# Kernel tuning notes

Hardware: AMD Instinct MI355X
Metric: run time of the kernel (lower is better)

Reference implementation:

```python
import jax, jax.numpy as jnp
import numpy as np

IMG = 160      # img_size
P = 100        # img_pathch_num = (160/16)^2
NBLK = 256     # pixels per 16x16 patch
NCLS = 4

def _index_matrix():
    # faithful port of NewAIFV.index_init
    ind = np.arange(256)
    start = (ind // 16) * IMG + (ind % 16) * 16
    idx = np.zeros(NBLK * P, dtype=np.int32)
    for i in range(P):
        idx[i * 256:(i + 1) * 256] = start + (i // 16) * 16 * IMG + (i % 16)
    return jnp.asarray(idx)

_IDX = _index_matrix()


def setup_inputs() -> dict:
    key = jax.random.key(0)
    ks = jax.random.split(key, 7)
    B, C = 4, 256
    return {
        "feat_S": jax.random.normal(ks[0], (B, C, IMG, IMG), jnp.float32),
        "feat_T": jax.random.normal(ks[1], (B, C, IMG, IMG), jnp.float32),
        "Pred_S": jax.random.normal(ks[2], (B, NCLS, IMG, IMG), jnp.float32),
        "Pred_T": jax.random.normal(ks[3], (B, NCLS, IMG, IMG), jnp.float32),
        "S_atten": jax.random.normal(ks[4], (B, P, P), jnp.float32),
        "T_atten": jax.random.normal(ks[5], (B, P, P), jnp.float32),
        "target": jax.random.randint(ks[6], (B, 1, IMG, IMG), 0, NCLS, jnp.int32),
    }


def _cos(a, b):
    # torch.nn.CosineSimilarity(dim=1): dot / max(|a||b|, 1e-8)
    num = (a * b).sum(1)
    den = jnp.maximum(jnp.sqrt((a * a).sum(1)) * jnp.sqrt((b * b).sum(1)), 1e-8)
    return num / den


def reference(feat_S, feat_T, Pred_S, Pred_T, S_atten, T_atten, target):
    B, C, H, W = feat_S.shape
    hw = H * W
    idx = _IDX
    # gathered patch reorder (index_select along flattened spatial dim)
    fS = feat_S.reshape(B, C, hw)[:, :, idx]
    fT = feat_T.reshape(B, C, hw)[:, :, idx]
    tg = target.reshape(B, 1, hw)[:, :, idx].reshape(B, 1, H, W)
    # 256-iteration loop of per-patch [B,C,100]@[B,100,100] matmuls -> one einsum
    TS = jnp.einsum('bcik,bkj->bcij', fS.reshape(B, C, NBLK, P), S_atten).reshape(B, C, H, W)
    TT = jnp.einsum('bcik,bkj->bcij', fT.reshape(B, C, NBLK, P), T_atten).reshape(B, C, H, W)
    ScS = jax.nn.softmax(Pred_S, axis=1).reshape(B, NCLS, hw)[:, :, idx].reshape(B, NCLS, H, W)
    ScT = jax.nn.softmax(Pred_T, axis=1).reshape(B, NCLS, hw)[:, :, idx].reshape(B, NCLS, H, W)
    dt = TS.dtype
    one_hot = (tg == jnp.arange(NCLS)[None, :, None, None]).astype(dt)   # [B,4,H,W]
    wei_s = (ScS * one_hot).sum(1)  # [B,H,W]
    wei_t = (ScT * one_hot).sum(1)
    tf = tg.astype(dt)  # [B,1,H,W], broadcast replaces nn.Upsample+expand

    def centers(class_list, s_prto, t_prto, eps):
        cS, cT = TS, TT
        for i in range(NCLS):
            j = class_list[i]
            stmp = ScT[:, j:j + 1]              # [B,1,H,W] (Score_Tmp, broadcast over C)
            m = (tf == i).astype(dt)            # mask_feat (class i)
            mp = (tf == j).astype(dt)           # mask_feat_prto (class class_list[i])
            denS = (mp if s_prto else m).sum((-1, -2)) + eps          # [B,1]
            protoS = ((mp * TS).sum((-1, -2)) / denS)[:, :, None, None]
            denT = (stmp * (mp if t_prto else m)).sum((-1, -2)) + eps
            protoT = ((mp * TT * stmp).sum((-1, -2)) / denT)[:, :, None, None]
            cS = (1 - m) * cS + m * protoS
            cT = (1 - m) * cT + m * protoT
        return cS, cT

    # three variants exactly as in the torch loops (denominator choices differ)
    cS0, cT0 = centers([1, 0, 3, 2], False, False, 1e-6)
    cS1, cT1 = centers([2, 3, 0, 1], True, True, 1e-6)
    cS2, cT2 = centers([3, 2, 1, 0], True, True, 1.0)

    w = (1 - wei_s) * wei_t
    vec_s = jnp.stack([w * _cos(TS, c) for c in (cS0, cS1, cS2)], axis=1)  # [B,3,H,W]
    vec_t = jnp.stack([w * _cos(TT, c) for c in (cT0, cT1, cT2)], axis=1)
    return jnp.mean((vec_s - vec_t) ** 2)
```

## Files before the change

kernel.cpp:

```cpp
#include <hip/hip_runtime.h>
#include <cstdint>
#include <cstddef>

#define HW 25600

typedef __attribute__((ext_vector_type(8))) short bf16x8;
typedef __attribute__((ext_vector_type(16))) float f32x16;

union ABu { bf16x8 v; uint2 u[2]; };
union B128 { bf16x8 v; int4 q; };

__device__ __forceinline__ f32x16 zero16() {
    f32x16 z;
#pragma unroll
    for (int i = 0; i < 16; ++i) z[i] = 0.f;
    return z;
}

__device__ __forceinline__ unsigned short f2bf(float x) {
    unsigned u = __builtin_bit_cast(unsigned, x);
    unsigned r = (u + 0x7FFF + ((u >> 16) & 1)) >> 16;
    return (unsigned short)r;
}

__device__ __forceinline__ float bf2f(unsigned short s) {
    return __builtin_bit_cast(float, (unsigned)s << 16);
}

__device__ __forceinline__ float wred(float v) {
#pragma unroll
    for (int off = 32; off; off >>= 1) v += __shfl_down(v, off, 64);
    return v;
}

__device__ double blockReduce256D(double v, double* s4) {
#pragma unroll
    for (int off = 32; off; off >>= 1) v += __shfl_down(v, off, 64);
    __syncthreads();
    if ((threadIdx.x & 63) == 0) s4[threadIdx.x >> 6] = v;
    __syncthreads();
    return s4[0] + s4[1] + s4[2] + s4[3];
}

__global__ __launch_bounds__(256) void k1_prep(
    const float* __restrict__ PredS, const float* __restrict__ PredT,
    const int* __restrict__ target,
    int* __restrict__ cls_arr, float* __restrict__ wT_arr,
    float* __restrict__ w_arr, float* __restrict__ partial_prep)
{
    __shared__ float sL[4][20];
    int blk = blockIdx.x;
    int b = blk / 100, r = blk - b * 100;
    int t = threadIdx.x, w = t >> 6, lane = t & 63;
    int ql = r * 256 + t;
    int v = ((t >> 4) * 160) + ((t & 15) * 16) + ((r >> 4) * 2560) + (r & 15);

    int cls = target[b * HW + v];

    const float* pS = PredS + b * 4 * HW + v;
    float a0 = pS[0], a1 = pS[HW], a2 = pS[2 * HW], a3 = pS[3 * HW];
    float mS = fmaxf(fmaxf(a0, a1), fmaxf(a2, a3));
    float e0 = expf(a0 - mS), e1 = expf(a1 - mS), e2 = expf(a2 - mS), e3 = expf(a3 - mS);
    float invS = 1.0f / (e0 + e1 + e2 + e3);
    float wei_s = ((cls == 0) ? e0 : (cls == 1) ? e1 : (cls == 2) ? e2 : e3) * invS;

    const float* pT = PredT + b * 4 * HW + v;
    float c0 = pT[0], c1 = pT[HW], c2 = pT[2 * HW], c3 = pT[3 * HW];
    float mT = fmaxf(fmaxf(c0, c1), fmaxf(c2, c3));
    float f0 = expf(c0 - mT), f1 = expf(c1 - mT), f2 = expf(c2 - mT), f3 = expf(c3 - mT);
    float invT = 1.0f / (f0 + f1 + f2 + f3);
    float tn0 = f0 * invT, tn1 = f1 * invT, tn2 = f2 * invT, tn3 = f3 * invT;
    float wei_t = (cls == 0) ? tn0 : (cls == 1) ? tn1 : (cls == 2) ? tn2 : tn3;

    cls_arr[b * HW + ql] = cls;
    wT_arr[b * HW + ql] = wei_t;
    w_arr[b * HW + ql] = (1.0f - wei_s) * wei_t;

    float vals[20];
#pragma unroll
    for (int s = 0; s < 4; ++s) vals[s] = (cls == s) ? 1.f : 0.f;
#pragma unroll
    for (int i2 = 0; i2 < 4; ++i2) {
        vals[4 + i2 * 4 + 0] = (cls == i2) ? tn0 : 0.f;
        vals[4 + i2 * 4 + 1] = (cls == i2) ? tn1 : 0.f;
        vals[4 + i2 * 4 + 2] = (cls == i2) ? tn2 : 0.f;
        vals[4 + i2 * 4 + 3] = (cls == i2) ? tn3 : 0.f;
    }
#pragma unroll
    for (int s = 0; s < 20; ++s) {
        float rv = wred(vals[s]);
        if (lane == 0) sL[w][s] = rv;
    }
    __syncthreads();
    if (t < 20) {
        int ob = blk * 20;
        partial_prep[ob + t] = sL[0][t] + sL[1][t] + sL[2][t] + sL[3][t];
    }
}

__global__ __launch_bounds__(128) void k2_w(
    const float* __restrict__ Satt, const float* __restrict__ Tatt,
    const int* __restrict__ cls_arr, const float* __restrict__ wT_arr,
    unsigned short* __restrict__ Wbf_S, unsigned short* __restrict__ Wbf_T,
    const float* __restrict__ partial_prep, float* __restrict__ cnt, float* __restrict__ E)
{
    int blk = blockIdx.x;
    int t = threadIdx.x;
    if (blk >= 1024) {
        int i = blk - 1024;
        if (t < 64) {
            int b = i / 20, s = i - (i / 20) * 20;
            float a = partial_prep[(b * 100 + t) * 20 + s];
            if (t + 64 < 100) a += partial_prep[(b * 100 + t + 64) * 20 + s];
            a = wred(a);
            if (t == 0) { if (s < 4) cnt[b * 4 + s] = a; else E[b * 16 + (s - 4)] = a; }
        }
        return;
    }
    __shared__ float Al[100 * 101];
    __shared__ int cls_s[100];
    __shared__ float wTs[100];
    int b = blk >> 8, i = blk & 255;
    if (t < 100) {
        cls_s[t] = cls_arr[b * HW + i * 100 + t];
        wTs[t] = wT_arr[b * HW + i * 100 + t];
    }
    for (int f = t; f < 10000; f += 128) Al[f + f / 100] = Satt[b * 10000 + f];
    __syncthreads();
    if (t < 100) {
        float a0 = 0, a1 = 0, a2 = 0, a3 = 0;
        for (int jc = 0; jc < 100; ++jc) {
            float a = Al[t * 101 + jc];
            int cc = cls_s[jc];
            a0 += (cc == 0) ? a : 0.f;
            a1 += (cc == 1) ? a : 0.f;
            a2 += (cc == 2) ? a : 0.f;
            a3 += (cc == 3) ? a : 0.f;
        }
        uint2 pk;
        pk.x = (unsigned)f2bf(a0) | ((unsigned)f2bf(a1) << 16);
        pk.y = (unsigned)f2bf(a2) | ((unsigned)f2bf(a3) << 16);
        *(uint2*)(Wbf_S + (size_t)(b * HW + i * 100 + t) * 4) = pk;
    }
    __syncthreads();
    for (int f = t; f < 10000; f += 128) Al[f + f / 100] = Tatt[b * 10000 + f];
    __syncthreads();
    if (t < 100) {
        float a0 = 0, a1 = 0, a2 = 0, a3 = 0;
        for (int jc = 0; jc < 100; ++jc) {
            float a = Al[t * 101 + jc] * wTs[jc];
            int cc = cls_s[jc];
            a0 += (cc == 0) ? a : 0.f;
            a1 += (cc == 1) ? a : 0.f;
            a2 += (cc == 2) ? a : 0.f;
            a3 += (cc == 3) ? a : 0.f;
        }
        uint2 pk;
        pk.x = (unsigned)f2bf(a0) | ((unsigned)f2bf(a1) << 16);
        pk.y = (unsigned)f2bf(a2) | ((unsigned)f2bf(a3) << 16);
        *(uint2*)(Wbf_T + (size_t)(b * HW + i * 100 + t) * 4) = pk;
    }
}

__global__ __launch_bounds__(256) void k3_scan(
    const float* __restrict__ featS, const float* __restrict__ featT,
    const unsigned short* __restrict__ WbfS, const unsigned short* __restrict__ WbfT,
    unsigned short* __restrict__ featP, float* __restrict__ pp)
{
    __shared__ unsigned short ldsW[16 * 260 + 8];
    __shared__ float sL[16];
    int x = blockIdx.x;
    int side = x & 1;
    int rest = x >> 1;
    int cq = rest & 63;
    int bd = rest >> 6;
    int D = bd % 7, b = bd / 7;
    int t = threadIdx.x, w = t >> 6, lane = t & 63;

    const float* feat = side ? featT : featS;
    const unsigned short* Wbf = side ? WbfT : WbfS;
    unsigned short* fP = featP + (size_t)side * 26214400u;
    int ppbase = side * 28672 + ((b * 7 + D) * 256) * 4;

    int nr = (D < 6) ? 2 : 1;
    bool act = !(D == 6 && t >= 128);

    int4 w4[2][4];
#pragma unroll
    for (int rep = 0; rep < 2; ++rep) {
        if (rep < nr && act) {
            int Pb = D * 4096 + rep * 2048 + t * 8;
            const int4* wp = (const int4*)(Wbf + ((size_t)b * HW + Pb) * 4);
            w4[rep][0] = wp[0]; w4[rep][1] = wp[1]; w4[rep][2] = wp[2]; w4[rep][3] = wp[3];
        }
    }

    for (int cv = 0; cv < 4; ++cv) {
        int c = cq * 4 + cv;
        const float* fbase = feat + (size_t)(b * 256 + c) * HW + 2560 * D;
#pragma unroll
        for (int ra = 0; ra < 4; ++ra) {
            int A = (t >> 6) + 4 * ra;
            int f4i = t & 63;
            float4 fx = *(const float4*)(fbase + 160 * A + 4 * f4i);
            uint2 pk;
            pk.x = (unsigned)f2bf(fx.x) | ((unsigned)f2bf(fx.y) << 16);
            pk.y = (unsigned)f2bf(fx.z) | ((unsigned)f2bf(fx.w) << 16);
            *(uint2*)(ldsW + A * 260 + 4 * f4i) = pk;
        }
        __syncthreads();

        float as0 = 0.f, as1 = 0.f, as2 = 0.f, as3 = 0.f;
        if (act) {
#pragma unroll
            for (int rep = 0; rep < 2; ++rep) {
                if (rep < nr) {
                    int Pb = D * 4096 + rep * 2048 + t * 8;
                    int A2 = (t & 31) >> 1;
                    int base_unit = A2 * 260 + 128 * (t & 1) + rep * 8 + (t >> 5);
                    unsigned short us[8];
                    float fv[8];
#pragma unroll
                    for (int e = 0; e < 8; ++e) {
                        us[e] = ldsW[base_unit + 16 * e];
                        fv[e] = bf2f(us[e]);
                    }
                    const unsigned short* ww = (const unsigned short*)w4[rep];
#pragma unroll
                    for (int e = 0; e < 8; ++e) {
                        as0 += fv[e] * bf2f(ww[e * 4 + 0]);
                        as1 += fv[e] * bf2f(ww[e * 4 + 1]);
                        as2 += fv[e] * bf2f(ww[e * 4 + 2]);
                        as3 += fv[e] * bf2f(ww[e * 4 + 3]);
                    }
                    int4 outp;
                    ((unsigned*)&outp)[0] = (unsigned)us[0] | ((unsigned)us[1] << 16);
                    ((unsigned*)&outp)[1] = (unsigned)us[2] | ((unsigned)us[3] << 16);
                    ((unsigned*)&outp)[2] = (unsigned)us[4] | ((unsigned)us[5] << 16);
                    ((unsigned*)&outp)[3] = (unsigned)us[6] | ((unsigned)us[7] << 16);
                    *(int4*)(fP + (size_t)(b * 256 + c) * HW + Pb) = outp;
                }
            }
        }

        float rv0 = wred(as0), rv1 = wred(as1), rv2 = wred(as2), rv3 = wred(as3);
        if (lane == 0) {
            sL[w * 4 + 0] = rv0; sL[w * 4 + 1] = rv1;
            sL[w * 4 + 2] = rv2; sL[w * 4 + 3] = rv3;
        }
        __syncthreads();
        if (t < 4) pp[ppbase + c * 4 + t] = sL[t] + sL[4 + t] + sL[8 + t] + sL[12 + t];
        __syncthreads();
    }
}

__global__ void k35_red(const float* __restrict__ pp, float* __restrict__ SumAll)
{
    int id = blockIdx.x * 256 + threadIdx.x;
    int side = id >> 12;
    int rem = id & 4095;
    int bc = rem >> 2, j = rem & 3;
    int b = bc >> 8, c = bc & 255;
    float a = 0.f;
    for (int D = 0; D < 7; ++D)
        a += pp[side * 28672 + (((b * 7 + D) * 256) + c) * 4 + j];
    SumAll[side * 4096 + bc * 4 + j] = a;
}

__global__ __launch_bounds__(256, 2) void k4_mfma(
    const unsigned short* __restrict__ featP,
    const float* __restrict__ SattG, const float* __restrict__ TattG,
    const float* __restrict__ SumAll,
    float* __restrict__ n2S, float* __restrict__ n2T,
    float* __restrict__ dotS, float* __restrict__ dotT)
{
    __shared__ __align__(16) unsigned short featL[32 * 408 + 16];
    __shared__ __align__(16) unsigned short attL[100 * 136];

    int x = blockIdx.x;
    int side = x & 1, chalf = (x >> 1) & 1, b = (x >> 2) & 3, g = x >> 4;
    int t = threadIdx.x, w = t >> 6, l = t & 63;

    const float* Att = side ? TattG : SattG;
    const float* Sum = SumAll + side * 4096;
    const unsigned short* fP = featP + (size_t)side * 26214400u;
    float* n2h = side ? n2T : n2S;
    float* doth = side ? dotT : dotS;

    for (int f = t; f < 13600; f += 256) attL[f] = 0;
    featL[(t >> 3) * 408 + 400 + (t & 7)] = 0;
    if (t < 16) featL[32 * 408 + t] = 0;
    __syncthreads();
    for (int f = t; f < 10000; f += 256) {
        int k = f / 100, j = f - k * 100;
        attL[j * 136 + k] = f2bf(Att[b * 10000 + f]);
    }
    __syncthreads();

    int lj = l & 31, lh = l >> 5;
    bf16x8 breg[7][4];
    {
        int j3 = 96 + lj; if (j3 > 99) j3 = 99;
        int rowoff[4] = { lj, 32 + lj, 64 + lj, j3 };
#pragma unroll
        for (int ks = 0; ks < 7; ++ks)
#pragma unroll
            for (int s = 0; s < 4; ++s)
                breg[ks][s] = ((const B128*)(attL + rowoff[s] * 136 + lh * 8 + ks * 16))->v;
    }

    float n2a[4] = {0, 0, 0, 0};
    float dota[4][4] = {};
    const unsigned short* arow = featL + lj * 408 + w * 100 + lh * 8;

#pragma unroll 1
    for (int ch = 0; ch < 4; ++ch) {
        __syncthreads();
        {
            const unsigned short* src = fP + (size_t)(b * 256 + chalf * 128 + ch * 32 + (t >> 3)) * HW
                                        + g * 400 + (t & 7) * 8;
            unsigned short* dst = featL + (t >> 3) * 408 + (t & 7) * 8;
#pragma unroll
            for (int i = 0; i < 7; ++i) {
                int cb = (t & 7) + i * 8;
                if (cb < 50)
                    *(int4*)(dst + i * 64) = *(const int4*)(src + i * 64);
            }
        }
        __syncthreads();

        f32x16 acc0 = zero16(), acc1 = zero16(), acc2 = zero16(), acc3 = zero16();
#pragma unroll
        for (int ks = 0; ks < 7; ++ks) {
            ABu aF;
            aF.u[0] = *(const uint2*)(arow + ks * 16);
            aF.u[1] = *(const uint2*)(arow + ks * 16 + 4);
            acc0 = __builtin_amdgcn_mfma_f32_32x32x16_bf16(aF.v, breg[ks][0], acc0, 0, 0, 0);
            acc1 = __builtin_amdgcn_mfma_f32_32x32x16_bf16(aF.v, breg[ks][1], acc1, 0, 0, 0);
            acc2 = __builtin_amdgcn_mfma_f32_32x32x16_bf16(aF.v, breg[ks][2], acc2, 0, 0, 0);
            acc3 = __builtin_amdgcn_mfma_f32_32x32x16_bf16(aF.v, breg[ks][3], acc3, 0, 0, 0);
        }

        int cb0 = chalf * 128 + ch * 32 + (lh << 2);
#pragma unroll
        for (int r = 0; r < 16; ++r) {
            int cl = (r & 3) + ((r >> 2) << 3);
            float4 sv = *(const float4*)(Sum + (size_t)(b * 256 + cb0 + cl) * 4);
            float v;
            v = acc0[r]; n2a[0] += v * v;
            dota[0][0] += v * sv.x; dota[0][1] += v * sv.y; dota[0][2] += v * sv.z; dota[0][3] += v * sv.w;
            v = acc1[r]; n2a[1] += v * v;
            dota[1][0] += v * sv.x; dota[1][1] += v * sv.y; dota[1][2] += v * sv.z; dota[1][3] += v * sv.w;
            v = acc2[r]; n2a[2] += v * v;
            dota[2][0] += v * sv.x; dota[2][1] += v * sv.y; dota[2][2] += v * sv.z; dota[2][3] += v * sv.w;
            v = acc3[r]; n2a[3] += v * v;
            dota[3][0] += v * sv.x; dota[3][1] += v * sv.y; dota[3][2] += v * sv.z; dota[3][3] += v * sv.w;
        }
    }

#pragma unroll
    for (int nt = 0; nt < 4; ++nt) {
        n2a[nt] += __shfl_down(n2a[nt], 32, 64);
#pragma unroll
        for (int m = 0; m < 4; ++m) dota[nt][m] += __shfl_down(dota[nt][m], 32, 64);
    }
    if (l < 32) {
        int i0 = g * 4 + w;
        int pqb = b * HW + i0 * 100;
#pragma unroll
        for (int nt = 0; nt < 4; ++nt) {
            int j = nt * 32 + l;
            if (j < 100) {
                n2h[chalf * 102400 + pqb + j] = n2a[nt];
                float4 dv = {dota[nt][0], dota[nt][1], dota[nt][2], dota[nt][3]};
                *(float4*)(doth + chalf * 409600 + (size_t)(pqb + j) * 4) = dv;
            }
        }
    }
}

__global__ void k45_tbl(const float* __restrict__ SumTS, const float* __restrict__ SumTT,
                        const float* __restrict__ cnt, const float* __restrict__ E,
                        float* __restrict__ tbl)
{
    int blk = blockIdx.x, t = threadIdx.x;
    if (blk < 32) {
        int b = blk >> 3, sj = blk & 7, stv = sj >> 2, j = sj & 3;
        const float* S = stv ? SumTT : SumTS;
        float s = 0.f;
#pragma unroll
        for (int u = 0; u < 4; ++u) {
            float xx = S[(b * 256 + t * 4 + u) * 4 + j];
            s += xx * xx;
        }
        s = wred(s);
        if (t == 0) tbl[b * 32 + stv * 4 + j] = sqrtf(s);
    } else if (t < 16) {
        int b = t >> 2, i = t & 3;
        tbl[b * 32 + 8 + 0 * 4 + i] = cnt[b * 4 + i] + 1e-6f;
        tbl[b * 32 + 8 + 1 * 4 + i] = cnt[b * 4 + (i ^ 2)] + 1e-6f;
        tbl[b * 32 + 8 + 2 * 4 + i] = cnt[b * 4 + (i ^ 3)] + 1.0f;
        tbl[b * 32 + 20 + 0 * 4 + i] = E[b * 16 + i * 4 + (i ^ 1)] + 1e-6f;
        tbl[b * 32 + 20 + 1 * 4 + i] = E[b * 16 + 5 * (i ^ 2)] + 1e-6f;
        tbl[b * 32 + 20 + 2 * 4 + i] = E[b * 16 + 5 * (i ^ 3)] + 1.0f;
    }
}

__global__ __launch_bounds__(256) void k5_final(
    const int* __restrict__ cls_arr, const float* __restrict__ w_arr,
    const float* __restrict__ n2S, const float* __restrict__ n2T,
    const float* __restrict__ dotS, const float* __restrict__ dotT,
    const float* __restrict__ tbl, double* __restrict__ partial_res)
{
    __shared__ double s4[4];
    int blk = blockIdx.x;
    int b = blk / 100, r = blk - b * 100;
    int t = threadIdx.x;
    int pq = b * HW + r * 256 + t;

    int i = cls_arr[pq];
    float wv = w_arr[pq];
    float sqS = sqrtf(n2S[pq] + n2S[102400 + pq]);
    float sqT = sqrtf(n2T[pq] + n2T[102400 + pq]);
    float4 dSa = *(const float4*)(dotS + (size_t)pq * 4);
    float4 dSb = *(const float4*)(dotS + 409600 + (size_t)pq * 4);
    float4 dTa = *(const float4*)(dotT + (size_t)pq * 4);
    float4 dTb = *(const float4*)(dotT + 409600 + (size_t)pq * 4);
    float4 dS = {dSa.x + dSb.x, dSa.y + dSb.y, dSa.z + dSb.z, dSa.w + dSb.w};
    float4 dT = {dTa.x + dTb.x, dTa.y + dTb.y, dTa.z + dTb.z, dTa.w + dTb.w};
    const float* tb = tbl + b * 32;

    double acc = 0.0;
#pragma unroll
    for (int v = 0; v < 3; ++v) {
        int j = i ^ (v + 1);
        float dsj = (j == 0) ? dS.x : (j == 1) ? dS.y : (j == 2) ? dS.z : dS.w;
        float dtj = (j == 0) ? dT.x : (j == 1) ? dT.y : (j == 2) ? dT.z : dT.w;
        float cnS = tb[j], cnT = tb[4 + j];
        float denS = tb[8 + v * 4 + i], denT = tb[20 + v * 4 + i];
        float cs = (dsj / denS) / fmaxf(sqS * (cnS / denS), 1e-8f);
        float ct = (dtj / denT) / fmaxf(sqT * (cnT / denT), 1e-8f);
        float vs = wv * cs, vt = wv * ct;
        float d = vs - vt;
        acc += (double)d * (double)d;
    }
    double tot = blockReduce256D(acc, s4);
    if (t == 0) partial_res[blk] = tot;
}

__global__ __launch_bounds__(256) void k6_out(const double* __restrict__ partial_res,
                                              float* __restrict__ out)
{
    __shared__ double s4[4];
    int t = threadIdx.x;
    double v = (t < 200) ? (partial_res[t] + partial_res[t + 200]) : 0.0;
    double tot = blockReduce256D(v, s4);
    if (t == 0) out[0] = (float)(tot / 307200.0);
}

extern "C" void kernel_launch(void* const* d_in, const int* in_sizes, int n_in,
                              void* d_out, int out_size, void* d_ws, size_t ws_size,
                              hipStream_t stream)
{
    const float* feat_S  = (const float*)d_in[0];
    const float* feat_T  = (const float*)d_in[1];
    const float* Pred_S  = (const float*)d_in[2];
    const float* Pred_T  = (const float*)d_in[3];
    const float* S_atten = (const float*)d_in[4];
    const float* T_atten = (const float*)d_in[5];
    const int*   target  = (const int*)d_in[6];

    float* ws = (float*)d_ws;
    unsigned short* featP = (unsigned short*)d_ws;
    unsigned short* WbfS  = (unsigned short*)(ws + 26214400);
    unsigned short* WbfT  = (unsigned short*)(ws + 26419200);
    int*   cls_a = (int*)(ws + 26624000);
    float* wT_a  = ws + 26726400;
    float* w_a   = ws + 26828800;
    float* SumTS = ws + 26931200;
    float* SumTT = ws + 26935296;
    float* n2S   = ws + 26939392;
    float* n2T   = ws + 27144192;
    float* dotS  = ws + 27348992;
    float* dotT  = ws + 28168192;
    float* pprep = ws + 28987392;
    float* cnt   = ws + 28995392;
    float* E     = ws + 28995408;
    float* tbl   = ws + 28995472;
    double* pres = (double*)(ws + 28995600);
    float* ppart = ws + 28996400;

    k1_prep<<<400, 256, 0, stream>>>(Pred_S, Pred_T, target, cls_a, wT_a, w_a, pprep);
    k2_w<<<1104, 128, 0, stream>>>(S_atten, T_atten, cls_a, wT_a, WbfS, WbfT, pprep, cnt, E);
    k3_scan<<<3584, 256, 0, stream>>>(feat_S, feat_T, WbfS, WbfT, featP, ppart);
    k35_red<<<32, 256, 0, stream>>>(ppart, SumTS);
    k4_mfma<<<1024, 256, 0, stream>>>(featP, S_atten, T_atten, SumTS, n2S, n2T, dotS, dotT);
    k45_tbl<<<33, 64, 0, stream>>>(SumTS, SumTT, cnt, E, tbl);
    k5_final<<<400, 256, 0, stream>>>(cls_a, w_a, n2S, n2T, dotS, dotT, tbl, pres);
    k6_out<<<1, 256, 0, stream>>>(pres, (float*)d_out);
}
```

Baseline: 155.0 us.

## Load k3 feature tiles via direct global-to-LDS loads, one channel per block

The scan kernel now stages fp32 feature rows straight into shared memory with global_load_lds using an XOR swizzle, rather than loading through registers and converting to bf16 before the LDS store. Each block now handles a single channel instead of looping over four, so the grid is four times larger and per-channel barriers go away. The bf16 pack uses the hardware v_cvt_pk_bf16_f32 instruction. In exchange LDS use doubles (fp32 tile), the Wbf weight loads are repeated per channel instead of amortised over four, and rounding may differ slightly from the manual conversion.

```diff
diff --git a/kernel.cpp b/kernel.cpp
--- a/kernel.cpp
+++ b/kernel.cpp
@@ -167,24 +167,33 @@
     const unsigned short* __restrict__ WbfS, const unsigned short* __restrict__ WbfT,
     unsigned short* __restrict__ featP, float* __restrict__ pp)
 {
-    __shared__ unsigned short ldsW[16 * 260 + 8];
+    __shared__ __align__(16) float fL[16 * 256];
     __shared__ float sL[16];
     int x = blockIdx.x;
-    int side = x & 1;
-    int rest = x >> 1;
-    int cq = rest & 63;
-    int bd = rest >> 6;
+    int side = x / 7168;
+    int rest = x - side * 7168;
+    int c = rest & 255;
+    int bd = rest >> 8;
     int D = bd % 7, b = bd / 7;
-    int t = threadIdx.x, w = t >> 6, lane = t & 63;
+    int t = threadIdx.x, w = t >> 6, l = t & 63;
 
     const float* feat = side ? featT : featS;
     const unsigned short* Wbf = side ? WbfT : WbfS;
     unsigned short* fP = featP + (size_t)side * 26214400u;
-    int ppbase = side * 28672 + ((b * 7 + D) * 256) * 4;
+
+    const float* fbase = feat + (size_t)(b * 256 + c) * HW + 2560 * D;
+#pragma unroll
+    for (int ra = 0; ra < 4; ++ra) {
+        int A = w + 4 * ra;
+        const float* src = fbase + 160 * A + ((l ^ (A & 7)) << 2);
+        __builtin_amdgcn_global_load_lds(
+            (const __attribute__((address_space(1))) void*)src,
+            (__attribute__((address_space(3))) void*)(fL + A * 256),
+            16, 0, 0);
+    }
 
     int nr = (D < 6) ? 2 : 1;
     bool act = !(D == 6 && t >= 128);
-
     int4 w4[2][4];
 #pragma unroll
     for (int rep = 0; rep < 2; ++rep) {
@@ -195,62 +204,53 @@
         }
     }
 
-    for (int cv = 0; cv < 4; ++cv) {
-        int c = cq * 4 + cv;
-        const float* fbase = feat + (size_t)(b * 256 + c) * HW + 2560 * D;
-#pragma unroll
-        for (int ra = 0; ra < 4; ++ra) {
-            int A = (t >> 6) + 4 * ra;
-            int f4i = t & 63;
-            float4 fx = *(const float4*)(fbase + 160 * A + 4 * f4i);
-            uint2 pk;
-            pk.x = (unsigned)f2bf(fx.x) | ((unsigned)f2bf(fx.y) << 16);
-            pk.y = (unsigned)f2bf(fx.z) | ((unsigned)f2bf(fx.w) << 16);
-            *(uint2*)(ldsW + A * 260 + 4 * f4i) = pk;
-        }
-        __syncthreads();
-
-        float as0 = 0.f, as1 = 0.f, as2 = 0.f, as3 = 0.f;
-        if (act) {
-#pragma unroll
-            for (int rep = 0; rep < 2; ++rep) {
-                if (rep < nr) {
-                    int Pb = D * 4096 + rep * 2048 + t * 8;
-                    int A2 = (t & 31) >> 1;
-                    int base_unit = A2 * 260 + 128 * (t & 1) + rep * 8 + (t >> 5);
-                    unsigned short us[8];
-                    float fv[8];
-#pragma unroll
-                    for (int e = 0; e < 8; ++e) {
-                        us[e] = ldsW[base_unit + 16 * e];
-                        fv[e] = bf2f(us[e]);
-                    }
-                    const unsigned short* ww = (const unsigned short*)w4[rep];
-#pragma unroll
-                    for (int e = 0; e < 8; ++e) {
-                        as0 += fv[e] * bf2f(ww[e * 4 + 0]);
-                        as1 += fv[e] * bf2f(ww[e * 4 + 1]);
-                        as2 += fv[e] * bf2f(ww[e * 4 + 2]);
-                        as3 += fv[e] * bf2f(ww[e * 4 + 3]);
-                    }
-                    int4 outp;
-                    ((unsigned*)&outp)[0] = (unsigned)us[0] | ((unsigned)us[1] << 16);
-                    ((unsigned*)&outp)[1] = (unsigned)us[2] | ((unsigned)us[3] << 16);
-                    ((unsigned*)&outp)[2] = (unsigned)us[4] | ((unsigned)us[5] << 16);
-                    ((unsigned*)&outp)[3] = (unsigned)us[6] | ((unsigned)us[7] << 16);
-                    *(int4*)(fP + (size_t)(b * 256 + c) * HW + Pb) = outp;
+    __syncthreads();
+
+    float as0 = 0.f, as1 = 0.f, as2 = 0.f, as3 = 0.f;
+    int A2 = (t & 31) >> 1;
+    int rowb = A2 * 256;
+    int sw = A2 & 7;
+    int obase = 128 * (t & 1) + (t >> 5);
+    if (act) {
+#pragma unroll
+        for (int rep = 0; rep < 2; ++rep) {
+            if (rep < nr) {
+                float fv[8];
+#pragma unroll
+                for (int e = 0; e < 8; ++e) {
+                    int o = obase + 8 * rep + 16 * e;
+                    fv[e] = fL[rowb + (((o >> 2) ^ sw) << 2) + (o & 3)];
                 }
+                const unsigned short* ww = (const unsigned short*)w4[rep];
+#pragma unroll
+                for (int e = 0; e < 8; ++e) {
+                    as0 += fv[e] * bf2f(ww[e * 4 + 0]);
+                    as1 += fv[e] * bf2f(ww[e * 4 + 1]);
+                    as2 += fv[e] * bf2f(ww[e * 4 + 2]);
+                    as3 += fv[e] * bf2f(ww[e * 4 + 3]);
+                }
+                int4 outp;
+#pragma unroll
+                for (int pr = 0; pr < 4; ++pr) {
+                    unsigned rr;
+                    asm("v_cvt_pk_bf16_f32 %0, %1, %2"
+                        : "=v"(rr) : "v"(fv[2 * pr]), "v"(fv[2 * pr + 1]));
+                    ((unsigned*)&outp)[pr] = rr;
+                }
+                *(int4*)(fP + (size_t)(b * 256 + c) * HW + D * 4096 + rep * 2048 + t * 8) = outp;
             }
         }
-
-        float rv0 = wred(as0), rv1 = wred(as1), rv2 = wred(as2), rv3 = wred(as3);
-        if (lane == 0) {
-            sL[w * 4 + 0] = rv0; sL[w * 4 + 1] = rv1;
-            sL[w * 4 + 2] = rv2; sL[w * 4 + 3] = rv3;
-        }
-        __syncthreads();
-        if (t < 4) pp[ppbase + c * 4 + t] = sL[t] + sL[4 + t] + sL[8 + t] + sL[12 + t];
-        __syncthreads();
+    }
+
+    float rv0 = wred(as0), rv1 = wred(as1), rv2 = wred(as2), rv3 = wred(as3);
+    if (l == 0) {
+        sL[w * 4 + 0] = rv0; sL[w * 4 + 1] = rv1;
+        sL[w * 4 + 2] = rv2; sL[w * 4 + 3] = rv3;
+    }
+    __syncthreads();
+    if (t < 4) {
+        pp[side * 28672 + ((b * 7 + D) * 256 + c) * 4 + t] =
+            sL[t] + sL[4 + t] + sL[8 + t] + sL[12 + t];
     }
 }
 
@@ -492,7 +492,7 @@
 
     k1_prep<<<400, 256, 0, stream>>>(Pred_S, Pred_T, target, cls_a, wT_a, w_a, pprep);
     k2_w<<<1104, 128, 0, stream>>>(S_atten, T_atten, cls_a, wT_a, WbfS, WbfT, pprep, cnt, E);
-    k3_scan<<<3584, 256, 0, stream>>>(feat_S, feat_T, WbfS, WbfT, featP, ppart);
+    k3_scan<<<14336, 256, 0, stream>>>(feat_S, feat_T, WbfS, WbfT, featP, ppart);
     k35_red<<<32, 256, 0, stream>>>(ppart, SumTS);
     k4_mfma<<<1024, 256, 0, stream>>>(featP, S_atten, T_atten, SumTS, n2S, n2T, dotS, dotT);
     k45_tbl<<<33, 64, 0, stream>>>(SumTS, SumTT, cnt, E, tbl);
```

New measurement: 166.5 us. +7.4%, slower.
